# Kernel tuning notes

Hardware: AMD Instinct MI355X
Metric: run time of the kernel (lower is better)

## Reference

```python
import jax, jax.numpy as jnp
import numpy as np

M = 100000  # sparse rows
K = 100000  # sparse cols
N = 128     # dense feature dim
NNZ = 2000000


def setup_inputs() -> dict:
    key = jax.random.key(0)
    k1, k2, k3 = jax.random.split(key, 3)
    indices = jax.random.randint(k1, (2, NNZ), 0, K, dtype=jnp.int64)  # row 0 = rows, row 1 = cols
    values = jax.random.normal(k2, (NNZ,), dtype=jnp.float32)
    dense_mat = jax.random.normal(k3, (K, N), dtype=jnp.float32)
    return {"indices": indices, "values": values, "dense_mat": dense_mat}


def reference(indices, values, dense_mat):
    # sparse COO [M,K] @ dense [K,N] -> [M,N]
    rows = indices[0]
    cols = indices[1]
    # gather dense rows for each nnz, scale by value, scatter-add into output rows
    contrib = values[:, None] * dense_mat[cols]  # [nnz, N]
    out = jax.ops.segment_sum(contrib, rows, num_segments=M)  # [M, N]
    return out
```

## Files before the change

### kernel.cpp

```cpp
#include <hip/hip_runtime.h>

#define NCOLS 128
#define BROWS 128
#define CAP   3072
#define TILE  8192
#define OVCAP 65536


__global__ void __launch_bounds__(256)
bin_kernel(const int* __restrict__ rows, const int* __restrict__ cols,
           const float* __restrict__ vals, int nnz, int nbuck,
           int2* __restrict__ scratch, int* __restrict__ bcur,
           int3* __restrict__ ovlist, int* __restrict__ ovcur) {
    __shared__ int cnt[800];
    __shared__ int gbase[800];
    int tid = threadIdx.x;
    int tile_base = blockIdx.x * TILE;

    for (int i = tid; i < nbuck; i += 256) cnt[i] = 0;
    __syncthreads();

    int myrow[32];
#pragma unroll
    for (int j = 0; j < 32; ++j) {
        int idx = tile_base + j * 256 + tid;
        int r = (idx < nnz) ? rows[idx] : -1;
        myrow[j] = r;
        if (r >= 0) atomicAdd(&cnt[r >> 7], 1);
    }
    __syncthreads();

    for (int b = tid; b < nbuck; b += 256) {
        int c = cnt[b];
        gbase[b] = (c > 0) ? atomicAdd(&bcur[b], c) : 0;
    }
    __syncthreads();
    for (int i = tid; i < nbuck; i += 256) cnt[i] = 0;
    __syncthreads();

#pragma unroll
    for (int j = 0; j < 32; ++j) {
        int idx = tile_base + j * 256 + tid;
        int r = myrow[j];
        if (r < 0) continue;
        int b = r >> 7;
        int rank = atomicAdd(&cnt[b], 1);
        int pos = gbase[b] + rank;
        int c = cols[idx];
        int vbits = __float_as_int(vals[idx]);
        if (pos < CAP) {
            scratch[(size_t)b * CAP + pos] = make_int2(((r & 127) << 17) | c, vbits);
        } else {
            int o = atomicAdd(ovcur, 1);
            if (o < OVCAP) ovlist[o] = make_int3(r, c, vbits);
        }
    }
}

__global__ void __launch_bounds__(256)
sort_bucket_kernel(int2* __restrict__ scratch, const int* __restrict__ bcur,
                   int* __restrict__ row_start, int* __restrict__ row_end,
                   int M) {
    __shared__ int2 stage[CAP];
    __shared__ int cnt[BROWS];
    __shared__ int off[BROWS];
    int b = blockIdx.x;
    int tid = threadIdx.x;
    int n = bcur[b];
    if (n > CAP) n = CAP;
    size_t base = (size_t)b * CAP;

    for (int i = tid; i < n; i += 256) stage[i] = scratch[base + i];
    if (tid < BROWS) cnt[tid] = 0;
    __syncthreads();

    for (int i = tid; i < n; i += 256) atomicAdd(&cnt[stage[i].x >> 17], 1);
    __syncthreads();

    if (tid < BROWS) off[tid] = cnt[tid];
    __syncthreads();
    for (int s = 1; s < BROWS; s <<= 1) {
        int v = 0;
        if (tid < BROWS && tid >= s) v = off[tid - s];
        __syncthreads();
        if (tid < BROWS) off[tid] += v;
        __syncthreads();
    }

    if (tid < BROWS) {
        int r = b * BROWS + tid;
        int excl = off[tid] - cnt[tid];
        if (r < M) {
            row_start[r] = (int)(base + excl);
            row_end[r]   = (int)(base + off[tid]);
        }
        off[tid] = excl;
    }
    __syncthreads();

    for (int i = tid; i < n; i += 256) {
        int lr = stage[i].x >> 17;
        int p = atomicAdd(&off[lr], 1);
        scratch[base + p] = stage[i];
    }
}

__global__ void __launch_bounds__(256)
overflow_kernel(const int3* __restrict__ ovlist, const int* __restrict__ ovcur,
                const float* __restrict__ dense, float* __restrict__ out) {
    int n = *ovcur;
    if (n > OVCAP) n = OVCAP;
    int tid = blockIdx.x * blockDim.x + threadIdx.x;
    int nth = gridDim.x * blockDim.x;
    for (int e = tid >> 5; e < n; e += nth >> 5) {
        int3 t = ovlist[e];
        float v = __int_as_float(t.z);
        int chunk = tid & 31;
        const float4 d =
            reinterpret_cast<const float4*>(dense + (size_t)t.y * NCOLS)[chunk];
        float* o = out + (size_t)t.x * NCOLS + chunk * 4;
        atomicAdd(o + 0, v * d.x);
        atomicAdd(o + 1, v * d.y);
        atomicAdd(o + 2, v * d.z);
        atomicAdd(o + 3, v * d.w);
    }
}

__global__ void __launch_bounds__(256)
csr_spmm_kernel(const int* __restrict__ row_start, const int* __restrict__ row_end,
                const int2* __restrict__ spair, const float* __restrict__ dense,
                float* __restrict__ out, int M) {
    int wid = threadIdx.x >> 6;
    int lane = threadIdx.x & 63;
    int row = blockIdx.x * 4 + wid;
    if (row >= M) return;

    int start = row_start[row];
    int end = row_end[row];
    int p = lane >> 4;
    int ch = lane & 15;

    float4 acc0 = make_float4(0.f, 0.f, 0.f, 0.f);
    float4 acc1 = make_float4(0.f, 0.f, 0.f, 0.f);

    int kk = start + p;
    int c = 0;
    float v = 0.f;
    if (kk < end) {
        int2 t = spair[kk];
        c = t.x & 0x1FFFF;
        v = __int_as_float(t.y);
    }

    for (int k = start; k < end; k += 4) {
        int kn = k + 4 + p;
        int cn = 0;
        float vn = 0.f;
        if (kn < end) {
            int2 t = spair[kn];
            cn = t.x & 0x1FFFF;
            vn = __int_as_float(t.y);
        }
        const float4* drow =
            reinterpret_cast<const float4*>(dense) + (size_t)c * (NCOLS / 4);
        float4 d0 = drow[ch];
        float4 d1 = drow[ch + 16];
        acc0.x += v * d0.x;
        acc0.y += v * d0.y;
        acc0.z += v * d0.z;
        acc0.w += v * d0.w;
        acc1.x += v * d1.x;
        acc1.y += v * d1.y;
        acc1.z += v * d1.z;
        acc1.w += v * d1.w;
        c = cn;
        v = vn;
    }

#pragma unroll
    for (int off = 16; off <= 32; off <<= 1) {
        acc0.x += __shfl_xor(acc0.x, off, 64);
        acc0.y += __shfl_xor(acc0.y, off, 64);
        acc0.z += __shfl_xor(acc0.z, off, 64);
        acc0.w += __shfl_xor(acc0.w, off, 64);
        acc1.x += __shfl_xor(acc1.x, off, 64);
        acc1.y += __shfl_xor(acc1.y, off, 64);
        acc1.z += __shfl_xor(acc1.z, off, 64);
        acc1.w += __shfl_xor(acc1.w, off, 64);
    }

    if (p == 0) {
        float4* orow = reinterpret_cast<float4*>(out) + (size_t)row * (NCOLS / 4);
        orow[ch] = acc0;
        orow[ch + 16] = acc1;
    }
}

__global__ void __launch_bounds__(256)
hist_kernel(const int* __restrict__ rows, int* __restrict__ counts, int nnz) {
    int i = blockIdx.x * 256 + threadIdx.x;
    if (i < nnz) atomicAdd(&counts[rows[i]], 1);
}

__global__ void __launch_bounds__(256)
block_reduce_kernel(const int* __restrict__ counts, int* __restrict__ bsums,
                    int M) {
    __shared__ int lds[256];
    int b = blockIdx.x, t = threadIdx.x;
    int base = b * 1024 + t * 4;
    int s = 0;
#pragma unroll
    for (int j = 0; j < 4; ++j)
        if (base + j < M) s += counts[base + j];
    lds[t] = s;
    __syncthreads();
    for (int off = 128; off > 0; off >>= 1) {
        if (t < off) lds[t] += lds[t + off];
        __syncthreads();
    }
    if (t == 0) bsums[b] = lds[0];
}

__global__ void __launch_bounds__(1024)
scan_bsums_kernel(int* __restrict__ bsums, int NB) {
    __shared__ int lds[1024];
    int t = threadIdx.x;
    int x = (t < NB) ? bsums[t] : 0;
    lds[t] = x;
    __syncthreads();
    for (int off = 1; off < 1024; off <<= 1) {
        int v = (t >= off) ? lds[t - off] : 0;
        __syncthreads();
        lds[t] += v;
        __syncthreads();
    }
    if (t < NB) bsums[t] = lds[t] - x;
}

__global__ void __launch_bounds__(256)
offsets_kernel(const int* __restrict__ counts, const int* __restrict__ bsums,
               int* __restrict__ row_start, int* __restrict__ row_endx,
               int* __restrict__ cursor, int M, int nnz) {
    __shared__ int lds[256];
    int b = blockIdx.x, t = threadIdx.x;
    int base = b * 1024 + t * 4;
    int c0 = 0, c1 = 0, c2 = 0, c3 = 0;
    if (base + 0 < M) c0 = counts[base + 0];
    if (base + 1 < M) c1 = counts[base + 1];
    if (base + 2 < M) c2 = counts[base + 2];
    if (base + 3 < M) c3 = counts[base + 3];
    int s = c0 + c1 + c2 + c3;
    lds[t] = s;
    __syncthreads();
    for (int off = 1; off < 256; off <<= 1) {
        int v = (t >= off) ? lds[t - off] : 0;
        __syncthreads();
        lds[t] += v;
        __syncthreads();
    }
    int off0 = bsums[b] + lds[t] - s;
    int e0 = off0, e1 = off0 + c0, e2 = e1 + c1, e3 = e2 + c2;
    if (base + 0 < M) { row_start[base + 0] = e0; row_endx[base + 0] = e1; cursor[base + 0] = e0; }
    if (base + 1 < M) { row_start[base + 1] = e1; row_endx[base + 1] = e2; cursor[base + 1] = e1; }
    if (base + 2 < M) { row_start[base + 2] = e2; row_endx[base + 2] = e3; cursor[base + 2] = e2; }
    if (base + 3 < M) { row_start[base + 3] = e3; row_endx[base + 3] = e3 + c3; cursor[base + 3] = e3; }
}

__global__ void __launch_bounds__(256)
scatter_kernel(const int* __restrict__ rows, const int* __restrict__ cols,
               const float* __restrict__ vals, int* __restrict__ cursor,
               int2* __restrict__ spair, int nnz) {
    int i = blockIdx.x * 256 + threadIdx.x;
    if (i >= nnz) return;
    int r = rows[i];
    int pos = atomicAdd(&cursor[r], 1);
    spair[pos] = make_int2(cols[i] & 0x1FFFF, __float_as_int(vals[i]));
}

__global__ void __launch_bounds__(256)
spmm_atomic_kernel(const int* __restrict__ rows, const int* __restrict__ cols,
                   const float* __restrict__ vals, const float* __restrict__ dense,
                   float* __restrict__ out, int nnz) {
    long long tid = (long long)blockIdx.x * blockDim.x + threadIdx.x;
    int i = (int)(tid >> 5);
    int chunk = (int)(tid & 31);
    if (i >= nnz) return;
    int r = rows[i];
    int c = cols[i];
    float v = vals[i];
    const float4 d =
        reinterpret_cast<const float4*>(dense + (size_t)c * NCOLS)[chunk];
    float* o = out + (size_t)r * NCOLS + (size_t)chunk * 4;
    atomicAdd(o + 0, v * d.x);
    atomicAdd(o + 1, v * d.y);
    atomicAdd(o + 2, v * d.z);
    atomicAdd(o + 3, v * d.w);
}

extern "C" void kernel_launch(void* const* d_in, const int* in_sizes, int n_in,
                              void* d_out, int out_size, void* d_ws, size_t ws_size,
                              hipStream_t stream) {
    const int*   idx   = (const int*)d_in[0];
    const float* vals  = (const float*)d_in[1];
    const float* dense = (const float*)d_in[2];
    float*       out   = (float*)d_out;

    const int nnz = in_sizes[1];
    const int* rows = idx;
    const int* cols = idx + nnz;
    const int M = out_size / NCOLS;
    const int nbuck = (M + BROWS - 1) / BROWS;

    size_t o_scratch = 0;
    size_t o_ovlist  = o_scratch + (size_t)nbuck * CAP * 8;
    size_t o_bcur    = o_ovlist + (size_t)OVCAP * 12;
    size_t o_ovcur   = o_bcur + (size_t)nbuck * 4;
    size_t o_rs      = o_ovcur + 4;
    size_t o_re      = o_rs + (size_t)M * 4;
    size_t need_new  = o_re + (size_t)M * 4;

    if (need_new <= ws_size && nbuck <= 800) {
        char* ws = (char*)d_ws;
        int2* scratch   = (int2*)(ws + o_scratch);
        int3* ovlist    = (int3*)(ws + o_ovlist);
        int*  bcur      = (int*)(ws + o_bcur);
        int*  ovcur     = (int*)(ws + o_ovcur);
        int*  row_start = (int*)(ws + o_rs);
        int*  row_end   = (int*)(ws + o_re);

        hipMemsetAsync(bcur, 0, (size_t)(nbuck + 1) * 4, stream);
        int ntile = (nnz + TILE - 1) / TILE;
        bin_kernel<<<ntile, 256, 0, stream>>>(rows, cols, vals, nnz, nbuck,
                                              scratch, bcur, ovlist, ovcur);
        sort_bucket_kernel<<<nbuck, 256, 0, stream>>>(scratch, bcur, row_start,
                                                      row_end, M);
        csr_spmm_kernel<<<(M + 3) / 4, 256, 0, stream>>>(row_start, row_end,
                                                         scratch, dense, out, M);
        overflow_kernel<<<32, 256, 0, stream>>>(ovlist, ovcur, dense, out);
        return;
    }

    const int NB = (M + 1023) / 1024;
    size_t f_spair  = 0;
    size_t f_counts = f_spair + 2 * (size_t)nnz;
    size_t f_cursor = f_counts + (size_t)M;
    size_t f_rs     = f_cursor + (size_t)M;
    size_t f_re     = f_rs + (size_t)M;
    size_t f_bsums  = f_re + (size_t)M;
    size_t need_old = (f_bsums + (size_t)NB) * 4;

    if (need_old <= ws_size && NB <= 1024) {
        int* wsI = (int*)d_ws;
        int2* spair     = (int2*)(wsI + f_spair);
        int*  counts    = wsI + f_counts;
        int*  cursor    = wsI + f_cursor;
        int*  row_start = wsI + f_rs;
        int*  row_end   = wsI + f_re;
        int*  bsums     = wsI + f_bsums;

        hipMemsetAsync(counts, 0, (size_t)M * 4, stream);
        hist_kernel<<<(nnz + 255) / 256, 256, 0, stream>>>(rows, counts, nnz);
        block_reduce_kernel<<<NB, 256, 0, stream>>>(counts, bsums, M);
        scan_bsums_kernel<<<1, 1024, 0, stream>>>(bsums, NB);
        offsets_kernel<<<NB, 256, 0, stream>>>(counts, bsums, row_start, row_end,
                                               cursor, M, nnz);
        scatter_kernel<<<(nnz + 255) / 256, 256, 0, stream>>>(rows, cols, vals,
                                                              cursor, spair, nnz);
        csr_spmm_kernel<<<(M + 3) / 4, 256, 0, stream>>>(row_start, row_end,
                                                         spair, dense, out, M);
        return;
    }

    hipMemsetAsync(d_out, 0, (size_t)out_size * sizeof(float), stream);
    const long long total = (long long)nnz * 32;
    spmm_atomic_kernel<<<(int)((total + 255) / 256), 256, 0, stream>>>(
        rows, cols, vals, dense, out, nnz);
}
```

Measured before the change: 310.0 us.

## Stage binned entries in LDS for coalesced writes; widen SpMM nnz parallelism to eight

The bin kernel now computes a block-local prefix sum of bucket counts, places each entry into a shared-memory staging array ordered by bucket, then writes the staged entries out contiguously per bucket. Each output position's bucket is found with a binary search over the local offsets. This aims to turn scattered global writes into coalesced runs, at the cost of 64KB of LDS per block, a prefix scan and per-element binary searches. Separately, the CSR SpMM kernel processes eight nonzeros per wave instead of four, with each lane holding four float4 accumulators, which gives more loads in flight per row but more registers and an extra shuffle-reduction step.

```diff
diff --git a/kernel.cpp b/kernel.cpp
--- a/kernel.cpp
+++ b/kernel.cpp
@@ -4,18 +4,23 @@
 #define BROWS 128
 #define CAP   3072
 #define TILE  8192
+#define NBMAX 800
 #define OVCAP 65536
-
 
 __global__ void __launch_bounds__(256)
 bin_kernel(const int* __restrict__ rows, const int* __restrict__ cols,
            const float* __restrict__ vals, int nnz, int nbuck,
            int2* __restrict__ scratch, int* __restrict__ bcur,
            int3* __restrict__ ovlist, int* __restrict__ ovcur) {
-    __shared__ int cnt[800];
-    __shared__ int gbase[800];
+    __shared__ int2 stage[TILE];
+    __shared__ int cnt[NBMAX];
+    __shared__ int loff[NBMAX + 1];
+    __shared__ int gbase[NBMAX];
+    __shared__ int ssum[256];
     int tid = threadIdx.x;
     int tile_base = blockIdx.x * TILE;
+    int tile_n = nnz - tile_base;
+    if (tile_n > TILE) tile_n = TILE;
 
     for (int i = tid; i < nbuck; i += 256) cnt[i] = 0;
     __syncthreads();
@@ -30,29 +35,65 @@
     }
     __syncthreads();
 
+    int b4 = tid * 4;
+    int c0 = 0, c1 = 0, c2 = 0, c3 = 0;
+    if (b4 + 0 < nbuck) c0 = cnt[b4 + 0];
+    if (b4 + 1 < nbuck) c1 = cnt[b4 + 1];
+    if (b4 + 2 < nbuck) c2 = cnt[b4 + 2];
+    if (b4 + 3 < nbuck) c3 = cnt[b4 + 3];
+    int s = c0 + c1 + c2 + c3;
+    ssum[tid] = s;
+    __syncthreads();
+    for (int st = 1; st < 256; st <<= 1) {
+        int v = (tid >= st) ? ssum[tid - st] : 0;
+        __syncthreads();
+        ssum[tid] += v;
+        __syncthreads();
+    }
+    int excl = ssum[tid] - s;
+    if (b4 + 0 < nbuck) loff[b4 + 0] = excl;
+    if (b4 + 1 < nbuck) loff[b4 + 1] = excl + c0;
+    if (b4 + 2 < nbuck) loff[b4 + 2] = excl + c0 + c1;
+    if (b4 + 3 < nbuck) loff[b4 + 3] = excl + c0 + c1 + c2;
+    if (tid == 0) loff[nbuck] = tile_n;
+    __syncthreads();
+
     for (int b = tid; b < nbuck; b += 256) {
-        int c = cnt[b];
-        gbase[b] = (c > 0) ? atomicAdd(&bcur[b], c) : 0;
-    }
-    __syncthreads();
-    for (int i = tid; i < nbuck; i += 256) cnt[i] = 0;
+        int cb = cnt[b];
+        gbase[b] = (cb > 0) ? atomicAdd(&bcur[b], cb) : 0;
+        cnt[b] = loff[b];
+    }
     __syncthreads();
 
 #pragma unroll
     for (int j = 0; j < 32; ++j) {
-        int idx = tile_base + j * 256 + tid;
         int r = myrow[j];
         if (r < 0) continue;
+        int idx = tile_base + j * 256 + tid;
         int b = r >> 7;
-        int rank = atomicAdd(&cnt[b], 1);
-        int pos = gbase[b] + rank;
-        int c = cols[idx];
-        int vbits = __float_as_int(vals[idx]);
+        int lp = atomicAdd(&cnt[b], 1);
+        stage[lp] = make_int2(((r & 127) << 17) | cols[idx],
+                              __float_as_int(vals[idx]));
+    }
+    __syncthreads();
+
+    for (int i = tid; i < tile_n; i += 256) {
+        int lo = 0, hi = nbuck;
+        while (hi - lo > 1) {
+            int mid = (lo + hi) >> 1;
+            if (loff[mid] <= i) lo = mid; else hi = mid;
+        }
+        int b = lo;
+        int pos = gbase[b] + (i - loff[b]);
+        int2 pr = stage[i];
         if (pos < CAP) {
-            scratch[(size_t)b * CAP + pos] = make_int2(((r & 127) << 17) | c, vbits);
+            scratch[(size_t)b * CAP + pos] = pr;
         } else {
             int o = atomicAdd(ovcur, 1);
-            if (o < OVCAP) ovlist[o] = make_int3(r, c, vbits);
+            if (o < OVCAP) {
+                int r = b * BROWS + (pr.x >> 17);
+                ovlist[o] = make_int3(r, pr.x & 0x1FFFF, pr.y);
+            }
         }
     }
 }
@@ -137,11 +178,13 @@
 
     int start = row_start[row];
     int end = row_end[row];
-    int p = lane >> 4;
-    int ch = lane & 15;
-
-    float4 acc0 = make_float4(0.f, 0.f, 0.f, 0.f);
-    float4 acc1 = make_float4(0.f, 0.f, 0.f, 0.f);
+    int p = lane >> 3;
+    int ch = lane & 7;
+
+    float4 a0 = make_float4(0.f, 0.f, 0.f, 0.f);
+    float4 a1 = make_float4(0.f, 0.f, 0.f, 0.f);
+    float4 a2 = make_float4(0.f, 0.f, 0.f, 0.f);
+    float4 a3 = make_float4(0.f, 0.f, 0.f, 0.f);
 
     int kk = start + p;
     int c = 0;
@@ -152,8 +195,8 @@
         v = __int_as_float(t.y);
     }
 
-    for (int k = start; k < end; k += 4) {
-        int kn = k + 4 + p;
+    for (int k = start; k < end; k += 8) {
+        int kn = k + 8 + p;
         int cn = 0;
         float vn = 0.f;
         if (kn < end) {
@@ -164,35 +207,35 @@
         const float4* drow =
             reinterpret_cast<const float4*>(dense) + (size_t)c * (NCOLS / 4);
         float4 d0 = drow[ch];
-        float4 d1 = drow[ch + 16];
-        acc0.x += v * d0.x;
-        acc0.y += v * d0.y;
-        acc0.z += v * d0.z;
-        acc0.w += v * d0.w;
-        acc1.x += v * d1.x;
-        acc1.y += v * d1.y;
-        acc1.z += v * d1.z;
-        acc1.w += v * d1.w;
+        float4 d1 = drow[ch + 8];
+        float4 d2 = drow[ch + 16];
+        float4 d3 = drow[ch + 24];
+        a0.x += v * d0.x; a0.y += v * d0.y; a0.z += v * d0.z; a0.w += v * d0.w;
+        a1.x += v * d1.x; a1.y += v * d1.y; a1.z += v * d1.z; a1.w += v * d1.w;
+        a2.x += v * d2.x; a2.y += v * d2.y; a2.z += v * d2.z; a2.w += v * d2.w;
+        a3.x += v * d3.x; a3.y += v * d3.y; a3.z += v * d3.z; a3.w += v * d3.w;
         c = cn;
         v = vn;
     }
 
 #pragma unroll
-    for (int off = 16; off <= 32; off <<= 1) {
-        acc0.x += __shfl_xor(acc0.x, off, 64);
-        acc0.y += __shfl_xor(acc0.y, off, 64);
-        acc0.z += __shfl_xor(acc0.z, off, 64);
-        acc0.w += __shfl_xor(acc0.w, off, 64);
-        acc1.x += __shfl_xor(acc1.x, off, 64);
-        acc1.y += __shfl_xor(acc1.y, off, 64);
-        acc1.z += __shfl_xor(acc1.z, off, 64);
-        acc1.w += __shfl_xor(acc1.w, off, 64);
+    for (int off = 8; off <= 32; off <<= 1) {
+        a0.x += __shfl_xor(a0.x, off, 64); a0.y += __shfl_xor(a0.y, off, 64);
+        a0.z += __shfl_xor(a0.z, off, 64); a0.w += __shfl_xor(a0.w, off, 64);
+        a1.x += __shfl_xor(a1.x, off, 64); a1.y += __shfl_xor(a1.y, off, 64);
+        a1.z += __shfl_xor(a1.z, off, 64); a1.w += __shfl_xor(a1.w, off, 64);
+        a2.x += __shfl_xor(a2.x, off, 64); a2.y += __shfl_xor(a2.y, off, 64);
+        a2.z += __shfl_xor(a2.z, off, 64); a2.w += __shfl_xor(a2.w, off, 64);
+        a3.x += __shfl_xor(a3.x, off, 64); a3.y += __shfl_xor(a3.y, off, 64);
+        a3.z += __shfl_xor(a3.z, off, 64); a3.w += __shfl_xor(a3.w, off, 64);
     }
 
     if (p == 0) {
         float4* orow = reinterpret_cast<float4*>(out) + (size_t)row * (NCOLS / 4);
-        orow[ch] = acc0;
-        orow[ch + 16] = acc1;
+        orow[ch] = a0;
+        orow[ch + 8] = a1;
+        orow[ch + 16] = a2;
+        orow[ch + 24] = a3;
     }
 }
 
@@ -319,7 +362,7 @@
     size_t o_re      = o_rs + (size_t)M * 4;
     size_t need_new  = o_re + (size_t)M * 4;
 
-    if (need_new <= ws_size && nbuck <= 800) {
+    if (need_new <= ws_size && nbuck <= NBMAX) {
         char* ws = (char*)d_ws;
         int2* scratch   = (int2*)(ws + o_scratch);
         int3* ovlist    = (int3*)(ws + o_ovlist);
```

Result: no change. 313.8 us (+1.2%).
